# Kernel tuning notes

Measured on AMD Instinct MI355X. Metric: run time of the kernel, lower is better.

Reference implementation:

```python
import jax, jax.numpy as jnp
import numpy as np

HIDDEN = 1024
HORIZON = 24
BATCH, SEQ, D_IN = 256, 512, 64


def setup_inputs() -> dict:
    key = jax.random.key(0)
    k1, k2, k3, k4, k5 = jax.random.split(key, 5)
    fan_in = D_IN + HIDDEN
    # flax Dense default: lecun_normal kernel, zero bias; use scaled normal
    W = jax.random.normal(k1, (fan_in, 4 * HIDDEN), jnp.float32) / np.sqrt(fan_in)
    b = jnp.zeros((4 * HIDDEN,), jnp.float32)
    Wout = jax.random.normal(k2, (HIDDEN, HORIZON), jnp.float32) / np.sqrt(HIDDEN)
    bout = jnp.zeros((HORIZON,), jnp.float32)
    x = jax.random.normal(k3, (BATCH, SEQ, D_IN), jnp.float32)
    return {"x": x, "W": W, "b": b, "Wout": Wout, "bout": bout}


def reference(x, W, b, Wout, bout):
    B, T, D = x.shape
    H = W.shape[1] // 4

    def step(carry, x_t):
        h, c = carry
        gates = jnp.concatenate([x_t, h], axis=-1) @ W + b  # [B, 4H]
        i, f, g, o = jnp.split(gates, 4, axis=-1)
        i = jax.nn.sigmoid(i)
        f = jax.nn.sigmoid(f)
        o = jax.nn.sigmoid(o)
        g = jnp.tanh(g)
        c = f * c + i * g
        h = o * jnp.tanh(c)
        return (h, c), None

    init = (jnp.zeros((B, H), x.dtype), jnp.zeros((B, H), x.dtype))
    (h_final, _), _ = jax.lax.scan(step, init, jnp.swapaxes(x, 0, 1))
    return h_final @ Wout + bout  # [B, horizon]
```

## Files before the change

kernel.cpp:

```cpp
#include <hip/hip_runtime.h>
#include <hip/hip_fp16.h>


#define T_STEPS 512
#define HID 1024
#define GRID 256
#define NTHR 512

typedef __attribute__((ext_vector_type(8))) _Float16 half8;
typedef __attribute__((ext_vector_type(4))) float f32x4;
typedef __attribute__((ext_vector_type(2))) float f32x2;

__device__ __forceinline__ float sigm(float v) { return 1.0f / (1.0f + __expf(-v)); }
__device__ __forceinline__ float tanh_fast(float v) { return 2.0f / (1.0f + __expf(-2.0f * v)) - 1.0f; }

__global__ void pack_w(const float* __restrict__ W, _Float16* __restrict__ Wp) {
    int idx = blockIdx.x * 256 + threadIdx.x;
    const int total = 64 * 136 * 64;
    if (idx >= total) return;
    int col = idx & 63;
    int kb = (idx >> 6) % 136;
    int n = (idx >> 6) / 136;
    int oc = ((col & 3) << 10) + (n << 4) + (col >> 2);
    const float* src = W + (size_t)(kb * 8) * 4096 + oc;
    _Float16* dst = Wp + (size_t)idx * 8;
#pragma unroll
    for (int j = 0; j < 8; j++) dst[j] = (_Float16)src[(size_t)j * 4096];
}

__global__ void __launch_bounds__(NTHR, 2) lstm_persist(
    const float* __restrict__ x,
    const _Float16* __restrict__ Wp,
    const float* __restrict__ bias,
    _Float16* __restrict__ hbuf,
    float* __restrict__ hfinal,
    unsigned int* bar)
{
    __shared__ float P[4 * 64 * 64];

    int wg = blockIdx.x;
    int xcd = wg & 7, slot = wg >> 3;
    int n = (xcd << 3) + (slot & 7);
    int m = slot >> 3;
    int B0 = m << 6;

    int tid = threadIdx.x;
    int wave = tid >> 6;
    int lane = tid & 63;
    int l15 = lane & 15, l4 = lane >> 4;
    int bb = tid & 63;
    int u0 = tid >> 6;

    float breg[2][4];
#pragma unroll
    for (int q = 0; q < 2; q++) {
        int u = (u0 << 1) + q;
#pragma unroll
        for (int g = 0; g < 4; g++) breg[q][g] = bias[(g << 10) + (n << 4) + u];
    }

    float cst[2] = {0.f, 0.f};

    const size_t HB = (size_t)128 * 256 * 8;
    const _Float16* WpBase = Wp + (size_t)n * 136 * 64 * 8;

    int hc[4];
#pragma unroll
    for (int j = 0; j < 4; j++) hc[j] = (wave < 2) ? (wave + 8 * (j + 1)) : (wave + 8 * j);
    half8 wfr[4][4];
#pragma unroll
    for (int j = 0; j < 4; j++) {
        int kb = (hc[j] << 2) + l4;
        const _Float16* wp = WpBase + ((size_t)kb << 9);
#pragma unroll
        for (int nn = 0; nn < 4; nn++) wfr[j][nn] = *(const half8*)(wp + (((nn << 4) + l15) << 3));
    }

    f32x4 acc[4][4];
#pragma unroll
    for (int i = 0; i < 4; i++)
#pragma unroll
        for (int j = 0; j < 4; j++) acc[i][j] = (f32x4){0.f, 0.f, 0.f, 0.f};

    auto XPREP = [&](int tt) {
        if (wave < 2) {
            int kb = (wave << 2) + l4;
            half8 bx[4];
            const _Float16* wp = WpBase + ((size_t)kb << 9);
#pragma unroll
            for (int nn = 0; nn < 4; nn++) bx[nn] = *(const half8*)(wp + (((nn << 4) + l15) << 3));
#pragma unroll
            for (int mm = 0; mm < 4; mm++) {
                const float* xp = x + ((size_t)(B0 + (mm << 4) + l15) * T_STEPS + tt) * 64 + (kb << 3);
                f32x4 lo = *(const f32x4*)xp;
                f32x4 hi = *(const f32x4*)(xp + 4);
                half8 v;
                v[0] = (_Float16)lo[0]; v[1] = (_Float16)lo[1];
                v[2] = (_Float16)lo[2]; v[3] = (_Float16)lo[3];
                v[4] = (_Float16)hi[0]; v[5] = (_Float16)hi[1];
                v[6] = (_Float16)hi[2]; v[7] = (_Float16)hi[3];
#pragma unroll
                for (int nn = 0; nn < 4; nn++)
                    acc[mm][nn] = __builtin_amdgcn_mfma_f32_16x16x32_f16(v, bx[nn], acc[mm][nn], 0, 0, 0);
            }
        }
    };

    XPREP(0);

    for (int t = 0; t < T_STEPS; t++) {
        const _Float16* cur = hbuf + (size_t)(t & 1) * HB;
        _Float16* nxt = hbuf + (size_t)((t + 1) & 1) * HB;

        half8 ah[4][4];
#pragma unroll
        for (int j = 0; j < 4; j++) {
            int kb = (hc[j] << 2) + l4;
            unsigned long long* hp =
                (unsigned long long*)(cur + (((size_t)(kb - 8) << 8) + B0 + l15) * 8);
#pragma unroll
            for (int mm = 0; mm < 4; mm++) {
                union { unsigned long long u[2]; half8 h; } cv;
                cv.u[0] = __hip_atomic_load(hp + (mm << 5), __ATOMIC_RELAXED, __HIP_MEMORY_SCOPE_AGENT);
                cv.u[1] = __hip_atomic_load(hp + (mm << 5) + 1, __ATOMIC_RELAXED, __HIP_MEMORY_SCOPE_AGENT);
                ah[j][mm] = cv.h;
            }
        }
#pragma unroll
        for (int j = 0; j < 4; j++)
#pragma unroll
            for (int mm = 0; mm < 4; mm++)
#pragma unroll
                for (int nn = 0; nn < 4; nn++)
                    acc[mm][nn] = __builtin_amdgcn_mfma_f32_16x16x32_f16(ah[j][mm], wfr[j][nn],
                                                                         acc[mm][nn], 0, 0, 0);

        if (wave < 4) {
#pragma unroll
            for (int mm = 0; mm < 4; mm++)
#pragma unroll
                for (int nn = 0; nn < 4; nn++) {
                    int c = (nn << 4) + l15;
                    int bblk = (mm << 2) + l4;
                    int word = (((wave << 6) + c) << 6) + (((bblk ^ l15) & 15) << 2);
                    *(f32x4*)&P[word] = acc[mm][nn];
                }
        }
        __syncthreads();
        if (wave >= 4) {
            int pw = wave - 4;
#pragma unroll
            for (int mm = 0; mm < 4; mm++)
#pragma unroll
                for (int nn = 0; nn < 4; nn++) {
                    int c = (nn << 4) + l15;
                    int bblk = (mm << 2) + l4;
                    int word = (((pw << 6) + c) << 6) + (((bblk ^ l15) & 15) << 2);
                    f32x4 v = *(f32x4*)&P[word];
                    v += acc[mm][nn];
                    *(f32x4*)&P[word] = v;
                }
        }
        __syncthreads();

        union { _Float16 h2[2]; unsigned int u; } hs;
        float hvf[2];
#pragma unroll
        for (int q = 0; q < 2; q++) {
            int u = (u0 << 1) + q;
            float g4[4];
#pragma unroll
            for (int g = 0; g < 4; g++) {
                int c = (u << 2) + g;
                int word = (c << 6) + (((((bb >> 2) ^ c) & 15) << 2) | (bb & 3));
                float s = breg[q][g];
#pragma unroll
                for (int w = 0; w < 4; w++) s += P[(w << 12) + word];
                g4[g] = s;
            }
            float ig = sigm(g4[0]);
            float fg = sigm(g4[1]);
            float gg = tanh_fast(g4[2]);
            float og = sigm(g4[3]);
            float cv = fg * cst[q] + ig * gg;
            cst[q] = cv;
            float hv = og * tanh_fast(cv);
            hs.h2[q] = (_Float16)hv;
            hvf[q] = hv;
        }
        int ug0 = (n << 4) + (u0 << 1);
        {
            unsigned int* dst =
                (unsigned int*)(nxt + ((size_t)(ug0 >> 3) * 256 + B0 + bb) * 8 + (ug0 & 7));
            __hip_atomic_store(dst, hs.u, __ATOMIC_RELAXED, __HIP_MEMORY_SCOPE_AGENT);
        }
        if (t == T_STEPS - 1) {
            f32x2 hv2; hv2[0] = hvf[0]; hv2[1] = hvf[1];
            *(f32x2*)&hfinal[(size_t)(B0 + bb) * HID + ug0] = hv2;
            break;
        }

        asm volatile("s_waitcnt vmcnt(0)" ::: "memory");
        __syncthreads();
        if (tid == 0)
            __hip_atomic_store(bar + (wg << 4), (unsigned int)(t + 1), __ATOMIC_RELAXED,
                               __HIP_MEMORY_SCOPE_AGENT);
#pragma unroll
        for (int i = 0; i < 4; i++)
#pragma unroll
            for (int j = 0; j < 4; j++) acc[i][j] = (f32x4){0.f, 0.f, 0.f, 0.f};
        XPREP(t + 1);
        if (tid >= 256) {
            const unsigned int* ap = bar + ((tid - 256) << 4);
            while (__hip_atomic_load(ap, __ATOMIC_RELAXED, __HIP_MEMORY_SCOPE_AGENT) <
                   (unsigned int)(t + 1)) {
                __builtin_amdgcn_s_sleep(1);
            }
        }
        __syncthreads();
    }
}

__global__ void proj_kernel(const float* __restrict__ hfinal, const float* __restrict__ Wout,
                            const float* __restrict__ bout, float* __restrict__ out) {
    int b = blockIdx.x;
    int l = threadIdx.x;
    float acc[24];
#pragma unroll
    for (int j = 0; j < 24; j++) acc[j] = 0.f;
    for (int i = 0; i < 16; i++) {
        int k = i * 64 + l;
        float h = hfinal[(size_t)b * HID + k];
        const float* wr = Wout + (size_t)k * 24;
#pragma unroll
        for (int j = 0; j < 24; j++) acc[j] += h * wr[j];
    }
    __shared__ float red[24][65];
#pragma unroll
    for (int j = 0; j < 24; j++) red[j][l] = acc[j];
    __syncthreads();
    if (l < 24) {
        float s = bout[l];
#pragma unroll
        for (int i = 0; i < 64; i++) s += red[l][i];
        out[b * 24 + l] = s;
    }
}

extern "C" void kernel_launch(void* const* d_in, const int* in_sizes, int n_in,
                              void* d_out, int out_size, void* d_ws, size_t ws_size,
                              hipStream_t stream) {
    const float* x = (const float*)d_in[0];
    const float* W = (const float*)d_in[1];
    const float* b = (const float*)d_in[2];
    const float* Wout = (const float*)d_in[3];
    const float* bout = (const float*)d_in[4];
    float* out = (float*)d_out;

    char* ws = (char*)d_ws;
    _Float16* Wp = (_Float16*)ws;
    _Float16* hbuf = (_Float16*)(ws + 8912896);
    float* hfinal = (float*)(ws + 8912896 + 1048576);
    unsigned int* bar = (unsigned int*)(ws + 8912896 + 2097152);

    hipMemsetAsync(hbuf, 0, (size_t)128 * 256 * 8 * sizeof(_Float16), stream);
    hipMemsetAsync(bar, 0, 16384, stream);

    pack_w<<<(64 * 136 * 64 + 255) / 256, 256, 0, stream>>>(W, Wp);

    void* args[6];
    args[0] = (void*)&x;
    args[1] = (void*)&Wp;
    args[2] = (void*)&b;
    args[3] = (void*)&hbuf;
    args[4] = (void*)&hfinal;
    args[5] = (void*)&bar;
    hipLaunchCooperativeKernel((void*)lstm_persist, dim3(GRID), dim3(NTHR), args, 0, stream);

    proj_kernel<<<256, 64, 0, stream>>>(hfinal, Wout, bout, out);
}
```

Before: 3.689 ms.

## Use per-batch-group barriers, XCD-local mapping, and plain h loads

Workgroups are remapped so each batch group of 64 rows sits on a pair of XCDs. The global 256-way barrier is replaced by a 64-way barrier over only the workgroups sharing that batch group, polled by one wave with a wave-wide all-check and an acquire fence. The h-state reads switch from relaxed atomic 64-bit loads to plain 128-bit vector loads, interleaved with MFMAs per k-chunk. The x-projection moves to waves 2-3, and sigmoid/tanh use the hardware reciprocal. This cuts barrier fan-in and load overhead, at some risk to memory-ordering correctness for plain loads of data written by other workgroups.

```diff
diff --git a/kernel.cpp b/kernel.cpp
--- a/kernel.cpp
+++ b/kernel.cpp
@@ -11,8 +11,12 @@
 typedef __attribute__((ext_vector_type(4))) float f32x4;
 typedef __attribute__((ext_vector_type(2))) float f32x2;
 
-__device__ __forceinline__ float sigm(float v) { return 1.0f / (1.0f + __expf(-v)); }
-__device__ __forceinline__ float tanh_fast(float v) { return 2.0f / (1.0f + __expf(-2.0f * v)) - 1.0f; }
+__device__ __forceinline__ float sigm(float v) {
+    return __builtin_amdgcn_rcpf(1.0f + __expf(-v));
+}
+__device__ __forceinline__ float tanh_fast(float v) {
+    return 2.0f * __builtin_amdgcn_rcpf(1.0f + __expf(-2.0f * v)) - 1.0f;
+}
 
 __global__ void pack_w(const float* __restrict__ W, _Float16* __restrict__ Wp) {
     int idx = blockIdx.x * 256 + threadIdx.x;
@@ -39,10 +43,11 @@
     __shared__ float P[4 * 64 * 64];
 
     int wg = blockIdx.x;
-    int xcd = wg & 7, slot = wg >> 3;
-    int n = (xcd << 3) + (slot & 7);
-    int m = slot >> 3;
+    int xcd = wg & 7;
+    int m = xcd >> 1;
+    int n = ((xcd & 1) << 5) + (wg >> 3);
     int B0 = m << 6;
+    int barId = (m << 6) + n;
 
     int tid = threadIdx.x;
     int wave = tid >> 6;
@@ -64,13 +69,10 @@
     const size_t HB = (size_t)128 * 256 * 8;
     const _Float16* WpBase = Wp + (size_t)n * 136 * 64 * 8;
 
-    int hc[4];
-#pragma unroll
-    for (int j = 0; j < 4; j++) hc[j] = (wave < 2) ? (wave + 8 * (j + 1)) : (wave + 8 * j);
     half8 wfr[4][4];
 #pragma unroll
     for (int j = 0; j < 4; j++) {
-        int kb = (hc[j] << 2) + l4;
+        int kb = ((2 + wave + 8 * j) << 2) + l4;
         const _Float16* wp = WpBase + ((size_t)kb << 9);
 #pragma unroll
         for (int nn = 0; nn < 4; nn++) wfr[j][nn] = *(const half8*)(wp + (((nn << 4) + l15) << 3));
@@ -83,8 +85,8 @@
         for (int j = 0; j < 4; j++) acc[i][j] = (f32x4){0.f, 0.f, 0.f, 0.f};
 
     auto XPREP = [&](int tt) {
-        if (wave < 2) {
-            int kb = (wave << 2) + l4;
+        if (wave == 2 || wave == 3) {
+            int kb = ((wave - 2) << 2) + l4;
             half8 bx[4];
             const _Float16* wp = WpBase + ((size_t)kb << 9);
 #pragma unroll
@@ -112,28 +114,20 @@
         const _Float16* cur = hbuf + (size_t)(t & 1) * HB;
         _Float16* nxt = hbuf + (size_t)((t + 1) & 1) * HB;
 
-        half8 ah[4][4];
 #pragma unroll
         for (int j = 0; j < 4; j++) {
-            int kb = (hc[j] << 2) + l4;
-            unsigned long long* hp =
-                (unsigned long long*)(cur + (((size_t)(kb - 8) << 8) + B0 + l15) * 8);
-#pragma unroll
-            for (int mm = 0; mm < 4; mm++) {
-                union { unsigned long long u[2]; half8 h; } cv;
-                cv.u[0] = __hip_atomic_load(hp + (mm << 5), __ATOMIC_RELAXED, __HIP_MEMORY_SCOPE_AGENT);
-                cv.u[1] = __hip_atomic_load(hp + (mm << 5) + 1, __ATOMIC_RELAXED, __HIP_MEMORY_SCOPE_AGENT);
-                ah[j][mm] = cv.h;
-            }
-        }
-#pragma unroll
-        for (int j = 0; j < 4; j++)
+            int kb = ((2 + wave + 8 * j) << 2) + l4;
+            const _Float16* hp = cur + (((size_t)(kb - 8) << 8) + B0 + l15) * 8;
+            half8 ah[4];
+#pragma unroll
+            for (int mm = 0; mm < 4; mm++) ah[mm] = *(const half8*)(hp + (mm << 7));
 #pragma unroll
             for (int mm = 0; mm < 4; mm++)
 #pragma unroll
                 for (int nn = 0; nn < 4; nn++)
-                    acc[mm][nn] = __builtin_amdgcn_mfma_f32_16x16x32_f16(ah[j][mm], wfr[j][nn],
+                    acc[mm][nn] = __builtin_amdgcn_mfma_f32_16x16x32_f16(ah[mm], wfr[j][nn],
                                                                          acc[mm][nn], 0, 0, 0);
+        }
 
         if (wave < 4) {
 #pragma unroll
@@ -189,33 +183,42 @@
             hvf[q] = hv;
         }
         int ug0 = (n << 4) + (u0 << 1);
+        if (t == T_STEPS - 1) {
+            f32x2 hv2; hv2[0] = hvf[0]; hv2[1] = hvf[1];
+            *(f32x2*)&hfinal[(size_t)(B0 + bb) * HID + ug0] = hv2;
+            break;
+        }
         {
             unsigned int* dst =
                 (unsigned int*)(nxt + ((size_t)(ug0 >> 3) * 256 + B0 + bb) * 8 + (ug0 & 7));
             __hip_atomic_store(dst, hs.u, __ATOMIC_RELAXED, __HIP_MEMORY_SCOPE_AGENT);
         }
-        if (t == T_STEPS - 1) {
-            f32x2 hv2; hv2[0] = hvf[0]; hv2[1] = hvf[1];
-            *(f32x2*)&hfinal[(size_t)(B0 + bb) * HID + ug0] = hv2;
-            break;
-        }
 
         asm volatile("s_waitcnt vmcnt(0)" ::: "memory");
         __syncthreads();
-        if (tid == 0)
-            __hip_atomic_store(bar + (wg << 4), (unsigned int)(t + 1), __ATOMIC_RELAXED,
-                               __HIP_MEMORY_SCOPE_AGENT);
+
 #pragma unroll
         for (int i = 0; i < 4; i++)
 #pragma unroll
             for (int j = 0; j < 4; j++) acc[i][j] = (f32x4){0.f, 0.f, 0.f, 0.f};
         XPREP(t + 1);
-        if (tid >= 256) {
-            const unsigned int* ap = bar + ((tid - 256) << 4);
-            while (__hip_atomic_load(ap, __ATOMIC_RELAXED, __HIP_MEMORY_SCOPE_AGENT) <
-                   (unsigned int)(t + 1)) {
-                __builtin_amdgcn_s_sleep(1);
+
+        if (wave == 0) {
+            if (lane == 0)
+                __hip_atomic_store(bar + ((size_t)barId << 4), (unsigned int)(t + 1),
+                                   __ATOMIC_RELAXED, __HIP_MEMORY_SCOPE_AGENT);
+            const unsigned int* ap = bar + ((size_t)((m << 6) + lane) << 4);
+            bool done = false;
+            while (!__all(done)) {
+                if (!done) {
+                    unsigned int v =
+                        __hip_atomic_load(ap, __ATOMIC_RELAXED, __HIP_MEMORY_SCOPE_AGENT);
+                    done = (v >= (unsigned int)(t + 1));
+                }
+                if (!done) __builtin_amdgcn_s_sleep(1);
             }
+            __builtin_amdgcn_fence(__ATOMIC_ACQUIRE, "agent");
+            asm volatile("s_waitcnt vmcnt(0)" ::: "memory");
         }
         __syncthreads();
     }
```

New measurement: 4.144 ms. 1.12x slower.
